# Performance work log

Hardware: AMD Instinct MI355X
Metric: run time of the kernel (lower is better)

Reference implementation:

```python
import jax, jax.numpy as jnp
import numpy as np

D_MODEL = 1024
N_HEADS = 16
D_HEAD = D_MODEL // N_HEADS
BATCH = 4
SEQ = 2048
NEG_INF = -1e9  # finite large-negative; avoids NaNs on fully-masked rows under jit


def setup_inputs() -> dict:
    key = jax.random.key(0)
    ks = jax.random.split(key, 10)
    xav = np.sqrt(6.0 / (D_MODEL + D_MODEL))  # xavier_uniform bound
    def w(k):
        return jax.random.uniform(k, (D_MODEL, D_MODEL), jnp.float32, -xav, xav)
    return {
        "x": jax.random.normal(ks[0], (BATCH, SEQ, D_MODEL), jnp.float32),
        "attention_mask": jnp.tril(jnp.ones((SEQ, SEQ), jnp.int32)),  # causal: 0 => masked
        "key_padding_mask": jnp.zeros((BATCH, SEQ), jnp.bool_),  # True => masked
        "Wq": w(ks[1]), "bq": jnp.zeros((D_MODEL,), jnp.float32),
        "Wk": w(ks[2]), "bk": jnp.zeros((D_MODEL,), jnp.float32),
        "Wv": w(ks[3]), "bv": jnp.zeros((D_MODEL,), jnp.float32),
        "Wo": w(ks[4]), "bo": jnp.zeros((D_MODEL,), jnp.float32),
    }


def reference(x, attention_mask, key_padding_mask, Wq, bq, Wk, bk, Wv, bv, Wo, bo):
    b, s, d = x.shape
    scale = 1.0 / np.sqrt(D_HEAD)
    # torch Linear: x @ W.T + b
    def proj(W, bias):
        y = jnp.einsum('bsd,ed->bse', x, W) + bias
        return y.reshape(b, s, N_HEADS, D_HEAD).transpose(0, 2, 1, 3)  # (b,h,s,dh)
    q = proj(Wq, bq)
    k = proj(Wk, bk)
    v = proj(Wv, bv)
    scores = jnp.einsum('bhqd,bhkd->bhqk', q, k) * scale  # (b,h,s,s)
    scores = jnp.where(attention_mask[None, None] == 0, NEG_INF, scores)
    scores = jnp.where(key_padding_mask[:, None, None, :], NEG_INF, scores)
    attn = jax.nn.softmax(scores, axis=-1)
    out = jnp.einsum('bhqk,bhkd->bhqd', attn, v)  # (b,h,s,dh)
    out = out.transpose(0, 2, 1, 3).reshape(b, s, d)
    out = jnp.einsum('bsd,ed->bse', out, Wo) + bo
    return out
```

## Files before the change

kernel.cpp:

```cpp
#include <hip/hip_runtime.h>
#include <stdint.h>

typedef __bf16 bf16;
typedef __bf16 bf16x4 __attribute__((ext_vector_type(4)));
typedef __bf16 bf16x8 __attribute__((ext_vector_type(8)));
typedef float f32x4 __attribute__((ext_vector_type(4)));

typedef __attribute__((address_space(3))) uint32_t lds_u32_t;
typedef const __attribute__((address_space(1))) uint32_t glb_u32_t;

#define MFMA16(a, b, c) __builtin_amdgcn_mfma_f32_16x16x32_bf16((a), (b), (c), 0, 0, 0)

#if __has_builtin(__builtin_amdgcn_exp2f)
#define EXP2(x) __builtin_amdgcn_exp2f(x)
#else
#define EXP2(x) exp2f(x)
#endif

#define SEQ 2048
#define DMODEL 1024
#define NH 16
#define DH 64
#define MTOT 8192

#define KVB 64

#define VMW(n) asm volatile("s_waitcnt vmcnt(" #n ")" ::: "memory")
#define LGKM0()                                         \
  {                                                     \
    asm volatile("s_waitcnt lgkmcnt(0)" ::: "memory");  \
    __builtin_amdgcn_sched_barrier(0);                  \
  }
#define BARR()                                          \
  {                                                     \
    asm volatile("" ::: "memory");                      \
    __builtin_amdgcn_s_barrier();                       \
    asm volatile("" ::: "memory");                      \
  }

__global__ __launch_bounds__(256) void cvt_f32_bf16(const float* __restrict__ in,
                                                    bf16* __restrict__ out, int n) {
  int i = blockIdx.x * blockDim.x + threadIdx.x;
  int idx = i * 4;
  if (idx < n) {
    float4 v = *reinterpret_cast<const float4*>(in + idx);
    bf16x4 o;
    o[0] = (bf16)v.x; o[1] = (bf16)v.y; o[2] = (bf16)v.z; o[3] = (bf16)v.w;
    *reinterpret_cast<bf16x4*>(out + idx) = o;
  }
}

__global__ __launch_bounds__(256) void cvt_w4(const float* __restrict__ W0,
                                              const float* __restrict__ W1,
                                              const float* __restrict__ W2,
                                              const float* __restrict__ W3,
                                              bf16* __restrict__ o0, bf16* __restrict__ o1,
                                              bf16* __restrict__ o2, bf16* __restrict__ o3) {
  const float* in;
  bf16* out;
  switch (blockIdx.y) {
    case 0: in = W0; out = o0; break;
    case 1: in = W1; out = o1; break;
    case 2: in = W2; out = o2; break;
    default: in = W3; out = o3; break;
  }
  int idx = (blockIdx.x * 256 + threadIdx.x) * 4;
  float4 v = *reinterpret_cast<const float4*>(in + idx);
  bf16x4 o;
  o[0] = (bf16)v.x; o[1] = (bf16)v.y; o[2] = (bf16)v.z; o[3] = (bf16)v.w;
  *reinterpret_cast<bf16x4*>(out + idx) = o;
}

static __device__ __forceinline__ void stage16(const bf16* g, const bf16* l) {
  __builtin_amdgcn_global_load_lds((glb_u32_t*)g, (lds_u32_t*)l, 16, 0, 0);
}

static __device__ __forceinline__ bf16x8 frag_ld(const bf16* base, int row, int col) {
  uint32_t byte = ((uint32_t)(row * 64 + col) * 2u) ^ (uint32_t)((row & 7) << 4);
  return *reinterpret_cast<const bf16x8*>(reinterpret_cast<const char*>(base) + byte);
}

static __device__ __forceinline__ void gemm256(const bf16* __restrict__ A,
                                               const bf16* __restrict__ B, int m0, int n0,
                                               int w, int lane, bf16* As, bf16* Bs,
                                               f32x4 acc[4][4]) {
  const int wm = w >> 1, wn = w & 1;
  const int cA = lane & 15, gA = lane >> 4;
  const int r8 = lane >> 3;
  const int csw = ((lane & 7) ^ r8) << 3;

#define SA_(half, kk, buf)                                                         \
  {                                                                                \
    _Pragma("unroll") for (int i_ = 0; i_ < 2; ++i_) {                             \
      int ci_ = w * 2 + i_;                                                        \
      stage16(A + (size_t)(m0 + (half)*128 + ci_ * 8 + r8) * 1024 + (kk) + csw,    \
              As + (buf)*16384 + (half)*8192 + ci_ * 512);                         \
    }                                                                              \
  }
#define SB_(kk, buf)                                                               \
  {                                                                                \
    _Pragma("unroll") for (int i_ = 0; i_ < 2; ++i_) {                             \
      int ci_ = w * 2 + i_;                                                        \
      stage16(B + (size_t)(n0 + ci_ * 8 + r8) * 1024 + (kk) + csw,                 \
              Bs + (buf)*8192 + ci_ * 512);                                        \
    }                                                                              \
  }
#define CL3(x) ((x) < 16 ? (x) : (x)-3)
#define CL2(x) ((x) < 16 ? (x) : (x)-2)

  SA_(0, 0, 0)
  SA_(1, 0, 0)
  SB_(0, 0)
  SA_(0, 64, 1)
  VMW(2);
  BARR();

  int cur = 0, nxt = 1, nx2 = 2;
  bf16x8 aA[2][2], bB[4][2];

  for (int t = 0; t < 16; ++t) {
    const int bcur = t & 1;
    const bf16* Ac = As + cur * 16384;
    const bf16* Bc = Bs + bcur * 8192;

#pragma unroll
    for (int mi2 = 0; mi2 < 2; ++mi2)
#pragma unroll
      for (int ks = 0; ks < 2; ++ks)
        aA[mi2][ks] = frag_ld(Ac, wm * 64 + mi2 * 16 + cA, ks * 32 + gA * 8);
#pragma unroll
    for (int ni = 0; ni < 4; ++ni)
#pragma unroll
      for (int ks = 0; ks < 2; ++ks)
        bB[ni][ks] = frag_ld(Bc, wn * 64 + ni * 16 + cA, ks * 32 + gA * 8);

    SA_(1, CL3(t + 1) * 64, nxt)
    SB_(CL2(t + 1) * 64, bcur ^ 1)

    BARR();
    LGKM0();
    __builtin_amdgcn_s_setprio(1);
#pragma unroll
    for (int mi2 = 0; mi2 < 2; ++mi2)
#pragma unroll
      for (int ni = 0; ni < 4; ++ni) {
        acc[mi2][ni] = MFMA16(aA[mi2][0], bB[ni][0], acc[mi2][ni]);
        acc[mi2][ni] = MFMA16(aA[mi2][1], bB[ni][1], acc[mi2][ni]);
      }
    __builtin_amdgcn_s_setprio(0);
    BARR();

#pragma unroll
    for (int mi2 = 0; mi2 < 2; ++mi2)
#pragma unroll
      for (int ks = 0; ks < 2; ++ks)
        aA[mi2][ks] = frag_ld(Ac, wm * 64 + 32 + mi2 * 16 + cA, ks * 32 + gA * 8);

    SA_(0, CL3(t + 2) * 64, nx2)

    VMW(2);
    BARR();
    LGKM0();
    __builtin_amdgcn_s_setprio(1);
#pragma unroll
    for (int mi2 = 0; mi2 < 2; ++mi2)
#pragma unroll
      for (int ni = 0; ni < 4; ++ni) {
        acc[2 + mi2][ni] = MFMA16(aA[mi2][0], bB[ni][0], acc[2 + mi2][ni]);
        acc[2 + mi2][ni] = MFMA16(aA[mi2][1], bB[ni][1], acc[2 + mi2][ni]);
      }
    __builtin_amdgcn_s_setprio(0);
    BARR();

    const int r_ = cur; cur = nxt; nxt = nx2; nx2 = r_;
  }
#undef SA_
#undef SB_
#undef CL3
#undef CL2
}

__global__ __launch_bounds__(512, 2) void qkv_gemm(
    const bf16* __restrict__ X, const bf16* __restrict__ Wq, const bf16* __restrict__ Wk,
    const bf16* __restrict__ Wv, const float* __restrict__ bq, const float* __restrict__ bk,
    const float* __restrict__ bv, bf16* __restrict__ Qo, bf16* __restrict__ Ko,
    bf16* __restrict__ Vt) {
  __shared__ bf16 As[3 * 16384];
  __shared__ bf16 Bs[2 * 8192];
  const int tid = threadIdx.x;
  const int w = tid >> 6, lane = tid & 63;
  const int ysel = blockIdx.y >> 3;
  const int n0 = (blockIdx.y & 7) * 128;
  const int m0 = blockIdx.x * 256;
  const bf16* W = (ysel == 0) ? Wq : ((ysel == 1) ? Wk : Wv);
  const float* bias = (ysel == 0) ? bq : ((ysel == 1) ? bk : bv);

  f32x4 acc[4][4];
  const f32x4 fz = {0.f, 0.f, 0.f, 0.f};
#pragma unroll
  for (int i = 0; i < 4; ++i)
#pragma unroll
    for (int j = 0; j < 4; ++j) acc[i][j] = fz;

  gemm256(X, W, m0, n0, w, lane, As, Bs, acc);

  const int wm = w >> 1, wn = w & 1;
  const int cA = lane & 15, gA = lane >> 4;

  if (ysel == 2) {
#pragma unroll
    for (int mi = 0; mi < 4; ++mi)
#pragma unroll
      for (int ni = 0; ni < 4; ++ni) {
        int e = n0 + wn * 64 + ni * 16 + cA;
        int h = e >> 6, dh = e & 63;
        int m = m0 + wm * 64 + mi * 16 + gA * 4;
        int b = m >> 11, s = m & 2047;
        float bb = bias[e];
        f32x4 v = acc[mi][ni];
        bf16x4 o;
        o[0] = (bf16)(v[0] + bb); o[1] = (bf16)(v[1] + bb);
        o[2] = (bf16)(v[2] + bb); o[3] = (bf16)(v[3] + bb);
        *reinterpret_cast<bf16x4*>(Vt + ((size_t)((b * NH + h) * DH + dh)) * SEQ + s) = o;
      }
  } else {
    bf16* dst = (ysel == 0) ? Qo : Ko;
    const float qs = (ysel == 0) ? 0.125f * 1.44269504f : 1.0f;
#pragma unroll
    for (int mi = 0; mi < 4; ++mi)
#pragma unroll
      for (int ni = 0; ni < 4; ++ni) {
        int e = n0 + wn * 64 + ni * 16 + cA;
        int h = e >> 6, dh = e & 63;
        int m = m0 + wm * 64 + mi * 16 + gA * 4;
        int b = m >> 11, s = m & 2047;
        float bb = bias[e];
        f32x4 v = acc[mi][ni];
        size_t base = ((size_t)(b * NH + h) * SEQ + s) * DH + dh;
#pragma unroll
        for (int j = 0; j < 4; ++j) dst[base + (size_t)j * DH] = (bf16)((v[j] + bb) * qs);
      }
  }
}

__global__ __launch_bounds__(512, 2) void out_gemm(const bf16* __restrict__ A,
                                                   const bf16* __restrict__ Wo,
                                                   const float* __restrict__ bo,
                                                   float* __restrict__ Out) {
  __shared__ bf16 As[3 * 16384];
  __shared__ bf16 Bs[2 * 8192];
  const int tid = threadIdx.x;
  const int w = tid >> 6, lane = tid & 63;
  const int m0 = blockIdx.x * 256;
  const int n0 = blockIdx.y * 128;

  f32x4 acc[4][4];
  const f32x4 fz = {0.f, 0.f, 0.f, 0.f};
#pragma unroll
  for (int i = 0; i < 4; ++i)
#pragma unroll
    for (int j = 0; j < 4; ++j) acc[i][j] = fz;

  gemm256(A, Wo, m0, n0, w, lane, As, Bs, acc);

  const int wm = w >> 1, wn = w & 1;
  const int cA = lane & 15, gA = lane >> 4;
#pragma unroll
  for (int mi = 0; mi < 4; ++mi)
#pragma unroll
    for (int ni = 0; ni < 4; ++ni) {
      int e = n0 + wn * 64 + ni * 16 + cA;
      int m = m0 + wm * 64 + mi * 16 + gA * 4;
      float bb = bo[e];
      f32x4 v = acc[mi][ni];
#pragma unroll
      for (int j = 0; j < 4; ++j) Out[(size_t)(m + j) * DMODEL + e] = v[j] + bb;
    }
}

__global__ __launch_bounds__(256) void flash_attn(const bf16* __restrict__ Q,
                                                  const bf16* __restrict__ K,
                                                  const bf16* __restrict__ Vt,
                                                  bf16* __restrict__ O) {
  __shared__ bf16 Ks[2][KVB * DH];
  __shared__ bf16 Vs[2][DH * KVB];
  __shared__ bf16 Plds[4 * 32 * 72];
  const int tid = threadIdx.x;
  const int w = tid >> 6, lane = tid & 63;
  const int bh = blockIdx.x;
  const int y = blockIdx.y;
  const int cA = lane & 15, gA = lane >> 4;
  const int l8 = lane & 7, r8 = lane >> 3;
  const int sb = lane & 48;

  const bf16* Qp = Q + (size_t)bh * SEQ * DH;
  const bf16* Kp = K + (size_t)bh * SEQ * DH;
  const bf16* Vp = Vt + (size_t)bh * DH * SEQ;
  const int b = bh >> 4, h = bh & 15;

  const uint32_t swz = (uint32_t)(cA & 7) << 4;
  const uint32_t lo0 = (uint32_t)cA * 128 + (((uint32_t)gA * 16) ^ swz);
  const uint32_t lo1 = (uint32_t)cA * 128 + ((64u + (uint32_t)gA * 16) ^ swz);
  char* pbase = (char*)Plds + w * 4608;

#define STAGE_K(dst, kv)                                                          \
  {                                                                               \
    _Pragma("unroll") for (int i = 0; i < 2; ++i) {                               \
      int ci = w * 2 + i;                                                         \
      int r = ci * 8 + r8;                                                        \
      int c = ((l8 ^ (r & 7)) << 3);                                              \
      stage16(Kp + (size_t)((kv) + r) * DH + c, (dst) + ci * 512);                \
    }                                                                             \
  }
#define STAGE_V(dst, kv)                                                          \
  {                                                                               \
    _Pragma("unroll") for (int i = 0; i < 2; ++i) {                               \
      int ci = w * 2 + i;                                                         \
      int r = ci * 8 + r8;                                                        \
      int c = ((l8 ^ (r & 7)) << 3);                                              \
      stage16(Vp + (size_t)r * SEQ + (kv) + c, (dst) + ci * 512);                 \
    }                                                                             \
  }

  const f32x4 fz = {0.f, 0.f, 0.f, 0.f};

  for (int phase = 0; phase < 2; ++phase) {
    const int qt = phase ? y : (15 - y);
    const int nt = (qt + 1) * 2;
    const int q0w = qt * 128 + w * 32;
    const int qmax = q0w + 31;

    bf16x8 qf[2][2];
#pragma unroll
    for (int qp = 0; qp < 2; ++qp)
#pragma unroll
      for (int ks = 0; ks < 2; ++ks)
        qf[qp][ks] = *reinterpret_cast<const bf16x8*>(
            Qp + (size_t)(q0w + qp * 16 + cA) * DH + ks * 32 + gA * 8);

    f32x4 o_acc[2][4];
#pragma unroll
    for (int qp = 0; qp < 2; ++qp)
#pragma unroll
      for (int dt = 0; dt < 4; ++dt) o_acc[qp][dt] = fz;
    float m_s[2] = {-1e30f, -1e30f}, l_s[2] = {0.f, 0.f};

    int cur = 0;
    STAGE_K(Ks[0], 0)
    STAGE_V(Vs[0], 0)
    __syncthreads();

    for (int it = 0; it < nt; ++it) {
      const int kv = it * KVB;
      if (it + 1 < nt) {
        STAGE_K(Ks[cur ^ 1], kv + KVB)
        STAGE_V(Vs[cur ^ 1], kv + KVB)
      }
      if (kv <= qmax) {
        const char* kc = (const char*)&Ks[cur][0];
        const char* vc = (const char*)&Vs[cur][0];

        bf16x8 kfr[4][2];
#pragma unroll
        for (int kt = 0; kt < 4; ++kt) {
          kfr[kt][0] = *reinterpret_cast<const bf16x8*>(kc + lo0 + kt * 2048);
          kfr[kt][1] = *reinterpret_cast<const bf16x8*>(kc + lo1 + kt * 2048);
        }

        f32x4 s[4][2];
        __builtin_amdgcn_s_setprio(1);
#pragma unroll
        for (int kt = 0; kt < 4; ++kt)
#pragma unroll
          for (int qp = 0; qp < 2; ++qp) {
            s[kt][qp] = MFMA16(kfr[kt][0], qf[qp][0], fz);
            s[kt][qp] = MFMA16(kfr[kt][1], qf[qp][1], s[kt][qp]);
          }
        __builtin_amdgcn_s_setprio(0);

#pragma unroll
        for (int qp = 0; qp < 2; ++qp) {
          if (kv + 63 > q0w + qp * 16) {
            const int q = q0w + qp * 16 + cA;
#pragma unroll
            for (int kt = 0; kt < 4; ++kt) {
              const int kb = kv + kt * 16 + gA * 4;
#pragma unroll
              for (int j = 0; j < 4; ++j)
                if (kb + j > q) s[kt][qp][j] = -1e30f;
            }
          }
        }

#pragma unroll
        for (int qp = 0; qp < 2; ++qp) {
          float r =
              fmaxf(fmaxf(fmaxf(s[0][qp][0], s[0][qp][1]), fmaxf(s[0][qp][2], s[0][qp][3])),
                    fmaxf(fmaxf(s[1][qp][0], s[1][qp][1]), fmaxf(s[1][qp][2], s[1][qp][3])));
          float r2 =
              fmaxf(fmaxf(fmaxf(s[2][qp][0], s[2][qp][1]), fmaxf(s[2][qp][2], s[2][qp][3])),
                    fmaxf(fmaxf(s[3][qp][0], s[3][qp][1]), fmaxf(s[3][qp][2], s[3][qp][3])));
          r = fmaxf(r, r2);
          r = fmaxf(r, __shfl_xor(r, 16));
          r = fmaxf(r, __shfl_xor(r, 32));

          const float mo = m_s[qp];
          float mn = mo;
          if (!__all(r <= mo + 12.0f)) {
            mn = fmaxf(mo, r);
            m_s[qp] = mn;
            const float scl = EXP2(mo - mn);
            float sclr[4];
#pragma unroll
            for (int j = 0; j < 4; ++j) sclr[j] = __shfl(scl, sb | (4 * gA + j));
#pragma unroll
            for (int dt = 0; dt < 4; ++dt) {
              f32x4 t = o_acc[qp][dt];
              t[0] *= sclr[0]; t[1] *= sclr[1]; t[2] *= sclr[2]; t[3] *= sclr[3];
              o_acc[qp][dt] = t;
            }
            l_s[qp] *= scl;
          }

          float rs = 0.f;
#pragma unroll
          for (int kt = 0; kt < 4; ++kt) {
            float p0 = EXP2(s[kt][qp][0] - mn);
            float p1 = EXP2(s[kt][qp][1] - mn);
            float p2 = EXP2(s[kt][qp][2] - mn);
            float p3 = EXP2(s[kt][qp][3] - mn);
            s[kt][qp][0] = p0; s[kt][qp][1] = p1; s[kt][qp][2] = p2; s[kt][qp][3] = p3;
            rs += (p0 + p1) + (p2 + p3);
          }
          rs += __shfl_xor(rs, 16);
          rs += __shfl_xor(rs, 32);
          l_s[qp] += rs;

#pragma unroll
          for (int kt = 0; kt < 4; ++kt) {
            bf16x4 t;
            t[0] = (bf16)s[kt][qp][0]; t[1] = (bf16)s[kt][qp][1];
            t[2] = (bf16)s[kt][qp][2]; t[3] = (bf16)s[kt][qp][3];
            *reinterpret_cast<bf16x4*>(pbase + (qp * 16 + cA) * 144 + kt * 32 + gA * 8) = t;
          }
        }

        bf16x8 pf[2][2];
#pragma unroll
        for (int qp = 0; qp < 2; ++qp) {
          pf[qp][0] = *reinterpret_cast<const bf16x8*>(pbase + (qp * 16 + cA) * 144 + gA * 16);
          pf[qp][1] =
              *reinterpret_cast<const bf16x8*>(pbase + (qp * 16 + cA) * 144 + 64 + gA * 16);
        }

        __builtin_amdgcn_s_setprio(1);
#pragma unroll
        for (int dt = 0; dt < 4; ++dt) {
          bf16x8 vf0 = *reinterpret_cast<const bf16x8*>(vc + lo0 + dt * 2048);
          bf16x8 vf1 = *reinterpret_cast<const bf16x8*>(vc + lo1 + dt * 2048);
#pragma unroll
          for (int qp = 0; qp < 2; ++qp) {
            o_acc[qp][dt] = MFMA16(pf[qp][0], vf0, o_acc[qp][dt]);
            o_acc[qp][dt] = MFMA16(pf[qp][1], vf1, o_acc[qp][dt]);
          }
        }
        __builtin_amdgcn_s_setprio(0);
      }
      __syncthreads();
      cur ^= 1;
    }

#pragma unroll
    for (int qp = 0; qp < 2; ++qp) {
      const float li = 1.0f / l_s[qp];
      float lrow[4];
#pragma unroll
      for (int j = 0; j < 4; ++j) lrow[j] = __shfl(li, sb | (4 * gA + j));
#pragma unroll
      for (int dt = 0; dt < 4; ++dt) {
        const int dh = dt * 16 + cA;
#pragma unroll
        for (int j = 0; j < 4; ++j) {
          const int srow = q0w + qp * 16 + gA * 4 + j;
          O[((size_t)(b * SEQ + srow)) * DMODEL + h * DH + dh] =
              (bf16)(o_acc[qp][dt][j] * lrow[j]);
        }
      }
    }
    __syncthreads();
  }
}

extern "C" void kernel_launch(void* const* d_in, const int* in_sizes, int n_in, void* d_out,
                              int out_size, void* d_ws, size_t ws_size, hipStream_t stream) {
  const float* x = (const float*)d_in[0];
  const float* Wq = (const float*)d_in[3];
  const float* bq = (const float*)d_in[4];
  const float* Wk = (const float*)d_in[5];
  const float* bk = (const float*)d_in[6];
  const float* Wv = (const float*)d_in[7];
  const float* bv = (const float*)d_in[8];
  const float* Wo = (const float*)d_in[9];
  const float* bo = (const float*)d_in[10];
  float* out = (float*)d_out;

  char* ws = (char*)d_ws;
  bf16* xb = (bf16*)(ws + 0);
  bf16* wqb = (bf16*)(ws + 16777216);
  bf16* wkb = (bf16*)(ws + 18874368);
  bf16* wvb = (bf16*)(ws + 20971520);
  bf16* wob = (bf16*)(ws + 23068672);
  bf16* Qb = (bf16*)(ws + 25165824);
  bf16* Kb = (bf16*)(ws + 41943040);
  bf16* Vt = (bf16*)(ws + 58720256);
  bf16* Ab = xb;

  cvt_f32_bf16<<<8192, 256, 0, stream>>>(x, xb, MTOT * DMODEL);
  cvt_w4<<<dim3(1024, 4), 256, 0, stream>>>(Wq, Wk, Wv, Wo, wqb, wkb, wvb, wob);

  qkv_gemm<<<dim3(32, 24), 512, 0, stream>>>(xb, wqb, wkb, wvb, bq, bk, bv, Qb, Kb, Vt);
  flash_attn<<<dim3(64, 8), 256, 0, stream>>>(Qb, Kb, Vt, Ab);
  out_gemm<<<dim3(32, 8), 512, 0, stream>>>(Ab, wob, bo, out);
}
```

Baseline: 182.4 us.

## Shrink attention query tile to 64 rows, double grid, add occupancy hint

Each flash-attention block now handles a 64-row query tile (16 rows per wave) instead of 128, and the grid doubles to 64x16 with balanced tile pairing per block. This gives more blocks for load balance, removes per-iteration skip logic since every KV tile intersects the causal region, and shrinks the per-wave P buffer with XOR swizzling to avoid bank conflicts. Launch bounds request 4 blocks per CU. In exchange, each K/V tile staged into LDS is reused by half as many queries, which doubles K/V global traffic and synchronisation per unit of work.

```diff
diff --git a/kernel.cpp b/kernel.cpp
--- a/kernel.cpp
+++ b/kernel.cpp
@@ -278,13 +278,13 @@
     }
 }
 
-__global__ __launch_bounds__(256) void flash_attn(const bf16* __restrict__ Q,
-                                                  const bf16* __restrict__ K,
-                                                  const bf16* __restrict__ Vt,
-                                                  bf16* __restrict__ O) {
+__global__ __launch_bounds__(256, 4) void flash_attn(const bf16* __restrict__ Q,
+                                                     const bf16* __restrict__ K,
+                                                     const bf16* __restrict__ Vt,
+                                                     bf16* __restrict__ O) {
   __shared__ bf16 Ks[2][KVB * DH];
   __shared__ bf16 Vs[2][DH * KVB];
-  __shared__ bf16 Plds[4 * 32 * 72];
+  __shared__ bf16 Plds[4 * 16 * 64];
   const int tid = threadIdx.x;
   const int w = tid >> 6, lane = tid & 63;
   const int bh = blockIdx.x;
@@ -301,7 +301,7 @@
   const uint32_t swz = (uint32_t)(cA & 7) << 4;
   const uint32_t lo0 = (uint32_t)cA * 128 + (((uint32_t)gA * 16) ^ swz);
   const uint32_t lo1 = (uint32_t)cA * 128 + ((64u + (uint32_t)gA * 16) ^ swz);
-  char* pbase = (char*)Plds + w * 4608;
+  char* pb = (char*)Plds + w * 2048;
 
 #define STAGE_K(dst, kv)                                                          \
   {                                                                               \
@@ -325,25 +325,18 @@
   const f32x4 fz = {0.f, 0.f, 0.f, 0.f};
 
   for (int phase = 0; phase < 2; ++phase) {
-    const int qt = phase ? y : (15 - y);
-    const int nt = (qt + 1) * 2;
-    const int q0w = qt * 128 + w * 32;
-    const int qmax = q0w + 31;
-
-    bf16x8 qf[2][2];
-#pragma unroll
-    for (int qp = 0; qp < 2; ++qp)
-#pragma unroll
-      for (int ks = 0; ks < 2; ++ks)
-        qf[qp][ks] = *reinterpret_cast<const bf16x8*>(
-            Qp + (size_t)(q0w + qp * 16 + cA) * DH + ks * 32 + gA * 8);
-
-    f32x4 o_acc[2][4];
-#pragma unroll
-    for (int qp = 0; qp < 2; ++qp)
-#pragma unroll
-      for (int dt = 0; dt < 4; ++dt) o_acc[qp][dt] = fz;
-    float m_s[2] = {-1e30f, -1e30f}, l_s[2] = {0.f, 0.f};
+    const int qt = phase ? y : (31 - y);
+    const int nt = qt + 1;
+    const int q0w = qt * 64 + w * 16;
+
+    bf16x8 qf[2];
+    qf[0] = *reinterpret_cast<const bf16x8*>(Qp + (size_t)(q0w + cA) * DH + gA * 8);
+    qf[1] = *reinterpret_cast<const bf16x8*>(Qp + (size_t)(q0w + cA) * DH + 32 + gA * 8);
+
+    f32x4 o_acc[4];
+#pragma unroll
+    for (int dt = 0; dt < 4; ++dt) o_acc[dt] = fz;
+    float m_s = -1e30f, l_s = 0.f;
 
     int cur = 0;
     STAGE_K(Ks[0], 0)
@@ -356,135 +349,117 @@
         STAGE_K(Ks[cur ^ 1], kv + KVB)
         STAGE_V(Vs[cur ^ 1], kv + KVB)
       }
-      if (kv <= qmax) {
-        const char* kc = (const char*)&Ks[cur][0];
-        const char* vc = (const char*)&Vs[cur][0];
-
-        bf16x8 kfr[4][2];
+      const char* kc = (const char*)&Ks[cur][0];
+      const char* vc = (const char*)&Vs[cur][0];
+
+      bf16x8 kfr[4][2];
+#pragma unroll
+      for (int kt = 0; kt < 4; ++kt) {
+        kfr[kt][0] = *reinterpret_cast<const bf16x8*>(kc + lo0 + kt * 2048);
+        kfr[kt][1] = *reinterpret_cast<const bf16x8*>(kc + lo1 + kt * 2048);
+      }
+
+      f32x4 s[4];
+      __builtin_amdgcn_s_setprio(1);
+#pragma unroll
+      for (int kt = 0; kt < 4; ++kt) {
+        s[kt] = MFMA16(kfr[kt][0], qf[0], fz);
+        s[kt] = MFMA16(kfr[kt][1], qf[1], s[kt]);
+      }
+      __builtin_amdgcn_s_setprio(0);
+
+      if (it + 1 == nt) {
+        const int q = q0w + cA;
 #pragma unroll
         for (int kt = 0; kt < 4; ++kt) {
-          kfr[kt][0] = *reinterpret_cast<const bf16x8*>(kc + lo0 + kt * 2048);
-          kfr[kt][1] = *reinterpret_cast<const bf16x8*>(kc + lo1 + kt * 2048);
+          const int kb = kv + kt * 16 + gA * 4;
+#pragma unroll
+          for (int j = 0; j < 4; ++j)
+            if (kb + j > q) s[kt][j] = -1e30f;
         }
-
-        f32x4 s[4][2];
-        __builtin_amdgcn_s_setprio(1);
-#pragma unroll
-        for (int kt = 0; kt < 4; ++kt)
-#pragma unroll
-          for (int qp = 0; qp < 2; ++qp) {
-            s[kt][qp] = MFMA16(kfr[kt][0], qf[qp][0], fz);
-            s[kt][qp] = MFMA16(kfr[kt][1], qf[qp][1], s[kt][qp]);
-          }
-        __builtin_amdgcn_s_setprio(0);
-
-#pragma unroll
-        for (int qp = 0; qp < 2; ++qp) {
-          if (kv + 63 > q0w + qp * 16) {
-            const int q = q0w + qp * 16 + cA;
-#pragma unroll
-            for (int kt = 0; kt < 4; ++kt) {
-              const int kb = kv + kt * 16 + gA * 4;
-#pragma unroll
-              for (int j = 0; j < 4; ++j)
-                if (kb + j > q) s[kt][qp][j] = -1e30f;
-            }
-          }
+      }
+
+      float r =
+          fmaxf(fmaxf(fmaxf(s[0][0], s[0][1]), fmaxf(s[0][2], s[0][3])),
+                fmaxf(fmaxf(s[1][0], s[1][1]), fmaxf(s[1][2], s[1][3])));
+      float r2 =
+          fmaxf(fmaxf(fmaxf(s[2][0], s[2][1]), fmaxf(s[2][2], s[2][3])),
+                fmaxf(fmaxf(s[3][0], s[3][1]), fmaxf(s[3][2], s[3][3])));
+      r = fmaxf(r, r2);
+      r = fmaxf(r, __shfl_xor(r, 16));
+      r = fmaxf(r, __shfl_xor(r, 32));
+
+      const float mo = m_s;
+      float mn = mo;
+      if (!__all(r <= mo + 12.0f)) {
+        mn = fmaxf(mo, r);
+        m_s = mn;
+        const float scl = EXP2(mo - mn);
+        float sclr[4];
+#pragma unroll
+        for (int j = 0; j < 4; ++j) sclr[j] = __shfl(scl, sb | (4 * gA + j));
+#pragma unroll
+        for (int dt = 0; dt < 4; ++dt) {
+          f32x4 t = o_acc[dt];
+          t[0] *= sclr[0]; t[1] *= sclr[1]; t[2] *= sclr[2]; t[3] *= sclr[3];
+          o_acc[dt] = t;
         }
-
-#pragma unroll
-        for (int qp = 0; qp < 2; ++qp) {
-          float r =
-              fmaxf(fmaxf(fmaxf(s[0][qp][0], s[0][qp][1]), fmaxf(s[0][qp][2], s[0][qp][3])),
-                    fmaxf(fmaxf(s[1][qp][0], s[1][qp][1]), fmaxf(s[1][qp][2], s[1][qp][3])));
-          float r2 =
-              fmaxf(fmaxf(fmaxf(s[2][qp][0], s[2][qp][1]), fmaxf(s[2][qp][2], s[2][qp][3])),
-                    fmaxf(fmaxf(s[3][qp][0], s[3][qp][1]), fmaxf(s[3][qp][2], s[3][qp][3])));
-          r = fmaxf(r, r2);
-          r = fmaxf(r, __shfl_xor(r, 16));
-          r = fmaxf(r, __shfl_xor(r, 32));
-
-          const float mo = m_s[qp];
-          float mn = mo;
-          if (!__all(r <= mo + 12.0f)) {
-            mn = fmaxf(mo, r);
-            m_s[qp] = mn;
-            const float scl = EXP2(mo - mn);
-            float sclr[4];
-#pragma unroll
-            for (int j = 0; j < 4; ++j) sclr[j] = __shfl(scl, sb | (4 * gA + j));
-#pragma unroll
-            for (int dt = 0; dt < 4; ++dt) {
-              f32x4 t = o_acc[qp][dt];
-              t[0] *= sclr[0]; t[1] *= sclr[1]; t[2] *= sclr[2]; t[3] *= sclr[3];
-              o_acc[qp][dt] = t;
-            }
-            l_s[qp] *= scl;
-          }
-
-          float rs = 0.f;
-#pragma unroll
-          for (int kt = 0; kt < 4; ++kt) {
-            float p0 = EXP2(s[kt][qp][0] - mn);
-            float p1 = EXP2(s[kt][qp][1] - mn);
-            float p2 = EXP2(s[kt][qp][2] - mn);
-            float p3 = EXP2(s[kt][qp][3] - mn);
-            s[kt][qp][0] = p0; s[kt][qp][1] = p1; s[kt][qp][2] = p2; s[kt][qp][3] = p3;
-            rs += (p0 + p1) + (p2 + p3);
-          }
-          rs += __shfl_xor(rs, 16);
-          rs += __shfl_xor(rs, 32);
-          l_s[qp] += rs;
-
-#pragma unroll
-          for (int kt = 0; kt < 4; ++kt) {
-            bf16x4 t;
-            t[0] = (bf16)s[kt][qp][0]; t[1] = (bf16)s[kt][qp][1];
-            t[2] = (bf16)s[kt][qp][2]; t[3] = (bf16)s[kt][qp][3];
-            *reinterpret_cast<bf16x4*>(pbase + (qp * 16 + cA) * 144 + kt * 32 + gA * 8) = t;
-          }
-        }
-
-        bf16x8 pf[2][2];
-#pragma unroll
-        for (int qp = 0; qp < 2; ++qp) {
-          pf[qp][0] = *reinterpret_cast<const bf16x8*>(pbase + (qp * 16 + cA) * 144 + gA * 16);
-          pf[qp][1] =
-              *reinterpret_cast<const bf16x8*>(pbase + (qp * 16 + cA) * 144 + 64 + gA * 16);
-        }
-
-        __builtin_amdgcn_s_setprio(1);
-#pragma unroll
-        for (int dt = 0; dt < 4; ++dt) {
-          bf16x8 vf0 = *reinterpret_cast<const bf16x8*>(vc + lo0 + dt * 2048);
-          bf16x8 vf1 = *reinterpret_cast<const bf16x8*>(vc + lo1 + dt * 2048);
-#pragma unroll
-          for (int qp = 0; qp < 2; ++qp) {
-            o_acc[qp][dt] = MFMA16(pf[qp][0], vf0, o_acc[qp][dt]);
-            o_acc[qp][dt] = MFMA16(pf[qp][1], vf1, o_acc[qp][dt]);
-          }
-        }
-        __builtin_amdgcn_s_setprio(0);
-      }
+        l_s *= scl;
+      }
+
+      float rs = 0.f;
+#pragma unroll
+      for (int kt = 0; kt < 4; ++kt) {
+        float p0 = EXP2(s[kt][0] - mn);
+        float p1 = EXP2(s[kt][1] - mn);
+        float p2 = EXP2(s[kt][2] - mn);
+        float p3 = EXP2(s[kt][3] - mn);
+        s[kt][0] = p0; s[kt][1] = p1; s[kt][2] = p2; s[kt][3] = p3;
+        rs += (p0 + p1) + (p2 + p3);
+      }
+      rs += __shfl_xor(rs, 16);
+      rs += __shfl_xor(rs, 32);
+      l_s += rs;
+
+#pragma unroll
+      for (int kt = 0; kt < 4; ++kt) {
+        bf16x4 t;
+        t[0] = (bf16)s[kt][0]; t[1] = (bf16)s[kt][1];
+        t[2] = (bf16)s[kt][2]; t[3] = (bf16)s[kt][3];
+        *reinterpret_cast<bf16x4*>(
+            pb + cA * 128 + (((uint32_t)(kt * 32 + gA * 8)) ^ swz)) = t;
+      }
+
+      bf16x8 pf0 = *reinterpret_cast<const bf16x8*>(pb + cA * 128 + (((uint32_t)(gA * 16)) ^ swz));
+      bf16x8 pf1 =
+          *reinterpret_cast<const bf16x8*>(pb + cA * 128 + (((uint32_t)(64 + gA * 16)) ^ swz));
+
+      __builtin_amdgcn_s_setprio(1);
+#pragma unroll
+      for (int dt = 0; dt < 4; ++dt) {
+        bf16x8 vf0 = *reinterpret_cast<const bf16x8*>(vc + lo0 + dt * 2048);
+        bf16x8 vf1 = *reinterpret_cast<const bf16x8*>(vc + lo1 + dt * 2048);
+        o_acc[dt] = MFMA16(pf0, vf0, o_acc[dt]);
+        o_acc[dt] = MFMA16(pf1, vf1, o_acc[dt]);
+      }
+      __builtin_amdgcn_s_setprio(0);
+
       __syncthreads();
       cur ^= 1;
     }
 
-#pragma unroll
-    for (int qp = 0; qp < 2; ++qp) {
-      const float li = 1.0f / l_s[qp];
-      float lrow[4];
-#pragma unroll
-      for (int j = 0; j < 4; ++j) lrow[j] = __shfl(li, sb | (4 * gA + j));
-#pragma unroll
-      for (int dt = 0; dt < 4; ++dt) {
-        const int dh = dt * 16 + cA;
-#pragma unroll
-        for (int j = 0; j < 4; ++j) {
-          const int srow = q0w + qp * 16 + gA * 4 + j;
-          O[((size_t)(b * SEQ + srow)) * DMODEL + h * DH + dh] =
-              (bf16)(o_acc[qp][dt][j] * lrow[j]);
-        }
+    const float li = 1.0f / l_s;
+    float lrow[4];
+#pragma unroll
+    for (int j = 0; j < 4; ++j) lrow[j] = __shfl(li, sb | (4 * gA + j));
+#pragma unroll
+    for (int dt = 0; dt < 4; ++dt) {
+      const int dh = dt * 16 + cA;
+#pragma unroll
+      for (int j = 0; j < 4; ++j) {
+        const int srow = q0w + gA * 4 + j;
+        O[((size_t)(b * SEQ + srow)) * DMODEL + h * DH + dh] =
+            (bf16)(o_acc[dt][j] * lrow[j]);
       }
     }
     __syncthreads();
@@ -519,6 +494,6 @@
   cvt_w4<<<dim3(1024, 4), 256, 0, stream>>>(Wq, Wk, Wv, Wo, wqb, wkb, wvb, wob);
 
   qkv_gemm<<<dim3(32, 24), 512, 0, stream>>>(xb, wqb, wkb, wvb, bq, bk, bv, Qb, Kb, Vt);
-  flash_attn<<<dim3(64, 8), 256, 0, stream>>>(Qb, Kb, Vt, Ab);
+  flash_attn<<<dim3(64, 16), 256, 0, stream>>>(Qb, Kb, Vt, Ab);
   out_gemm<<<dim3(32, 8), 512, 0, stream>>>(Ab, wob, bo, out);
 }
```

After: 173.2 us. 1.05x faster.
